# Optimization experiments

Measured on AMD Instinct MI355X. Metric: run time of the kernel, lower is better.

The kernel has to match this reference:

```python
import jax, jax.numpy as jnp
import numpy as np

N, K, D = 32768, 8192, 256


def setup_inputs() -> dict:
    key = jax.random.key(0)
    k1, k2 = jax.random.split(key)
    z = jax.random.normal(k1, (N, D), dtype=jnp.float32)
    # nn.Embedding weight initialized uniform(-1/K, 1/K)
    emb = jax.random.uniform(k2, (K, D), dtype=jnp.float32, minval=-1.0 / K, maxval=1.0 / K)
    return {"z": z, "emb": emb}


def reference(z, emb):
    # squared-distance: ||z||^2 + ||e||^2 - 2 z e^T  -> [N, K]
    distances = (
        jnp.sum(z * z, axis=-1, keepdims=True)
        + jnp.sum(emb * emb, axis=-1)
        - 2.0 * (z @ emb.T)
    )
    closest = jnp.argmin(distances, axis=-1)  # [N]
    one_hot = jax.nn.one_hot(closest, emb.shape[0], dtype=z.dtype)  # [N, K]
    quantized = one_hot @ emb  # [N, D]
    return quantized
```

## Files before the change

kernel.cpp:

```cpp
#include <hip/hip_runtime.h>

#define NROWS 32768
#define KC 8192
#define DDIM 256
#define D4 64
#define CAP 128
#define DELTA 4e-4f

typedef _Float16 half8 __attribute__((ext_vector_type(8)));
typedef float f32x4 __attribute__((ext_vector_type(4)));
typedef unsigned int uint;
typedef const __attribute__((address_space(1))) unsigned int* gptr_u32;
typedef __attribute__((address_space(3))) unsigned int* lptr_u32;

union H4 { ushort4 u; _Float16 h[4]; };

__global__ __launch_bounds__(256) void vq_znorm(const float* __restrict__ z,
                                                float* __restrict__ An) {
#pragma clang fp contract(off)
  const int row = blockIdx.x * 256 + threadIdx.x;
  const float* a = z + (size_t)row * 256;
  float halves[2];
#pragma unroll
  for (int h = 0; h < 2; ++h) {
    const float* p = a + h * 128;
    float r[8];
#pragma unroll
    for (int j = 0; j < 8; ++j) { const float v = p[j]; r[j] = v * v; }
    for (int i = 8; i < 128; i += 8) {
#pragma unroll
      for (int j = 0; j < 8; ++j) { const float v = p[i + j]; r[j] += v * v; }
    }
    halves[h] = ((r[0] + r[1]) + (r[2] + r[3])) + ((r[4] + r[5]) + (r[6] + r[7]));
  }
  An[row] = halves[0] + halves[1];
}

__global__ __launch_bounds__(256) void vq_convert(const float* __restrict__ z,
                                                  const float* __restrict__ emb,
                                                  _Float16* __restrict__ z16,
                                                  _Float16* __restrict__ e16,
                                                  uint* __restrict__ rowmin,
                                                  int* __restrict__ cnt) {
  const int tid = blockIdx.x * 256 + threadIdx.x;
  const float4* z4 = (const float4*)z;
  const float4* e4 = (const float4*)emb;
  ushort4* z16u = (ushort4*)z16;
  ushort4* e16u = (ushort4*)e16;
#pragma unroll
  for (int t = 0; t < 4; ++t) {
    const int i = tid + t * 524288;
    const float4 v = z4[i];
    H4 o;
    o.h[0] = (_Float16)v.x; o.h[1] = (_Float16)v.y;
    o.h[2] = (_Float16)v.z; o.h[3] = (_Float16)v.w;
    z16u[i] = o.u;
  }
  {
    const int i = tid;
    const float4 v = e4[i];
    H4 o;
    o.h[0] = (_Float16)(v.x * 8192.0f); o.h[1] = (_Float16)(v.y * 8192.0f);
    o.h[2] = (_Float16)(v.z * 8192.0f); o.h[3] = (_Float16)(v.w * 8192.0f);
    e16u[i] = o.u;
  }
  if (tid < NROWS) { rowmin[tid] = 0x7F800000u; cnt[tid] = 0; }
}

__global__ __launch_bounds__(256) void vq_gemm_filter(
    const _Float16* __restrict__ z16, const _Float16* __restrict__ e16,
    const float* __restrict__ An, uint* __restrict__ rowmin,
    int* __restrict__ cnt, int* __restrict__ list) {
  __shared__ _Float16 As[128 * 32];
  __shared__ _Float16 Bs[128 * 32];
  const int bid = blockIdx.x;
  const int swz = (bid & 7) * 2048 + (bid >> 3);
  const int nIdx = swz >> 8;
  const int mIdx = swz & 255;
  const int brow = mIdx * 128, bcol = nIdx * 128;
  const int tid = threadIdx.x;
  const int lane = tid & 63, w = tid >> 6;
  const int wr = w >> 1, wc = w & 1;
  const int l15 = lane & 15, l4 = lane >> 4;

  f32x4 acc[4][4] = {{{0.f}}};

  for (int ks = 0; ks < 8; ++ks) {
    const int k0 = ks * 32;
    __syncthreads();
#pragma unroll
    for (int i = 0; i < 2; ++i) {
      const int c = tid + 256 * i;
      const int r = c >> 2, off = (c & 3) * 8;
      __builtin_amdgcn_global_load_lds(
          (gptr_u32)(z16 + (size_t)(brow + r) * DDIM + k0 + off),
          (lptr_u32)(As + c * 8), 16, 0, 0);
      __builtin_amdgcn_global_load_lds(
          (gptr_u32)(e16 + (size_t)(bcol + r) * DDIM + k0 + off),
          (lptr_u32)(Bs + c * 8), 16, 0, 0);
    }
    __syncthreads();
    half8 af[4], bf[4];
#pragma unroll
    for (int m = 0; m < 4; ++m)
      af[m] = *(const half8*)(As + (wr * 64 + m * 16 + l15) * 32 + l4 * 8);
#pragma unroll
    for (int n = 0; n < 4; ++n)
      bf[n] = *(const half8*)(Bs + (wc * 64 + n * 16 + l15) * 32 + l4 * 8);
#pragma unroll
    for (int m = 0; m < 4; ++m)
#pragma unroll
      for (int n = 0; n < 4; ++n)
        acc[m][n] = __builtin_amdgcn_mfma_f32_16x16x32_f16(af[m], bf[n], acc[m][n], 0, 0, 0);
  }

  float An_r[4][4];
#pragma unroll
  for (int m = 0; m < 4; ++m)
#pragma unroll
    for (int r = 0; r < 4; ++r)
      An_r[m][r] = An[brow + wr * 64 + m * 16 + l4 * 4 + r];

  float rmin[4][4];
#pragma unroll
  for (int m = 0; m < 4; ++m)
#pragma unroll
    for (int r = 0; r < 4; ++r) rmin[m][r] = 3.4e38f;
#pragma unroll
  for (int m = 0; m < 4; ++m)
#pragma unroll
    for (int n = 0; n < 4; ++n)
#pragma unroll
      for (int r = 0; r < 4; ++r) {
        const float s = fmaf(acc[m][n][r], -0x1p-12f, An_r[m][r]);
        acc[m][n][r] = s;
        rmin[m][r] = fminf(rmin[m][r], s);
      }
#pragma unroll
  for (int off = 1; off < 16; off <<= 1)
#pragma unroll
    for (int m = 0; m < 4; ++m)
#pragma unroll
      for (int r = 0; r < 4; ++r)
        rmin[m][r] = fminf(rmin[m][r], __shfl_xor(rmin[m][r], off, 64));

  float cur[4][4];
#pragma unroll
  for (int m = 0; m < 4; ++m)
#pragma unroll
    for (int r = 0; r < 4; ++r) {
      const int row = brow + wr * 64 + m * 16 + l4 * 4 + r;
      float oldf = 3.4e38f;
      if (l15 == 0)
        oldf = __uint_as_float(atomicMin(rowmin + row, __float_as_uint(rmin[m][r])));
      oldf = __shfl(oldf, lane & 48, 64);
      cur[m][r] = fminf(oldf, rmin[m][r]) + DELTA;
    }
#pragma unroll
  for (int m = 0; m < 4; ++m)
#pragma unroll
    for (int n = 0; n < 4; ++n)
#pragma unroll
      for (int r = 0; r < 4; ++r) {
        if (acc[m][n][r] <= cur[m][r]) {
          const int row = brow + wr * 64 + m * 16 + l4 * 4 + r;
          const int code = bcol + wc * 64 + n * 16 + l15;
          const int pos = atomicAdd(cnt + row, 1);
          if (pos < CAP) list[row * CAP + pos] = code;
        }
      }
}

__global__ __launch_bounds__(64) void vq_recheck(
    const float* __restrict__ z, const float* __restrict__ emb,
    const float* __restrict__ An, const int* __restrict__ cnt,
    const int* __restrict__ list, int* __restrict__ idxo) {
  const int row = blockIdx.x;
  const int lane = threadIdx.x;
  const int nc = cnt[row];
  const float Ar = An[row];
  const float4* z4r = (const float4*)z + (size_t)row * D4;
  const float4* e4 = (const float4*)emb;
  float bs = 3.4e38f;
  int bi = 0x7fffffff;
  if (nc <= CAP) {
    for (int c = lane; c < nc; c += 64) {
      const int code = list[row * CAP + c];
      float p = 0.f;
      for (int d = 0; d < D4; ++d) {
        const float4 zv = z4r[d];
        const float4 ev = e4[(size_t)code * D4 + d];
        p = fmaf(zv.x, ev.x, p); p = fmaf(zv.y, ev.y, p);
        p = fmaf(zv.z, ev.z, p); p = fmaf(zv.w, ev.w, p);
      }
      const float s = Ar - 2.0f * p;
      if (s < bs || (s == bs && code < bi)) { bs = s; bi = code; }
    }
  } else {
    for (int code = lane; code < KC; code += 64) {
      float p = 0.f;
      for (int d = 0; d < D4; ++d) {
        const float4 zv = z4r[d];
        const float4 ev = e4[(size_t)code * D4 + d];
        p = fmaf(zv.x, ev.x, p); p = fmaf(zv.y, ev.y, p);
        p = fmaf(zv.z, ev.z, p); p = fmaf(zv.w, ev.w, p);
      }
      const float s = Ar - 2.0f * p;
      if (s < bs || (s == bs && code < bi)) { bs = s; bi = code; }
    }
  }
#pragma unroll
  for (int off = 1; off < 64; off <<= 1) {
    const float os = __shfl_xor(bs, off, 64);
    const int oi = __shfl_xor(bi, off, 64);
    if (os < bs || (os == bs && oi < bi)) { bs = os; bi = oi; }
  }
  if (lane == 0) idxo[row] = bi;
}

__global__ __launch_bounds__(256) void vq_gather(const float* __restrict__ emb,
                                                 const int* __restrict__ idxo,
                                                 float* __restrict__ out) {
  const float4* e4 = (const float4*)emb;
  float4* o4 = (float4*)out;
  const int id = blockIdx.x * 256 + threadIdx.x;
#pragma unroll
  for (int t = 0; t < 4; ++t) {
    const int g = id + t * 524288;
    const int nrow = g >> 6;
    const int d4c = g & 63;
    o4[g] = e4[(size_t)idxo[nrow] * D4 + d4c];
  }
}

extern "C" void kernel_launch(void* const* d_in, const int* in_sizes, int n_in,
                              void* d_out, int out_size, void* d_ws, size_t ws_size,
                              hipStream_t stream) {
  const float* z = (const float*)d_in[0];
  const float* emb = (const float*)d_in[1];
  float* out = (float*)d_out;

  char* wsb = (char*)d_ws;
  float* An = (float*)(wsb);
  uint* rowmin = (uint*)(wsb + (128 << 10));
  int* cnt = (int*)(wsb + (256 << 10));
  int* idx = (int*)(wsb + (384 << 10));
  int* list = (int*)(wsb + (512 << 10));
  _Float16* z16 = (_Float16*)(wsb + (512 << 10) + (16 << 20));
  _Float16* e16 = (_Float16*)(wsb + (512 << 10) + (32 << 20));

  vq_znorm<<<NROWS / 256, 256, 0, stream>>>(z, An);
  vq_convert<<<2048, 256, 0, stream>>>(z, emb, z16, e16, rowmin, cnt);
  vq_gemm_filter<<<16384, 256, 0, stream>>>(z16, e16, An, rowmin, cnt, list);
  vq_recheck<<<NROWS, 64, 0, stream>>>(z, emb, An, cnt, list, idx);
  vq_gather<<<2048, 256, 0, stream>>>(emb, idx, out);
}
```

Before: 623.8 us.

## Keep z tile in registers and stream codebook panels with double-buffered LDS

The GEMM-filter kernel now keeps each block's full 128-row fp16 z tile (all 256 dims) in registers and loops over a 1024-code segment in 64-code panels. The panels are double-buffered in XOR-swizzled LDS, and each row's running minimum is tightened as panels go by, so fewer candidates get pushed to the lists. This replaces 16384 small blocks that each reloaded z and E over K with 2048 persistent blocks, which cuts global traffic and atomic contention. The recheck and gather kernels are fused so each wave writes its output row directly, and znorm switches to float4 loads; the cost is more registers and larger shared memory, which can lower occupancy.

```diff
diff --git a/kernel.cpp b/kernel.cpp
--- a/kernel.cpp
+++ b/kernel.cpp
@@ -6,6 +6,11 @@
 #define D4 64
 #define CAP 128
 #define DELTA 4e-4f
+#define MT 128
+#define NSEG 8
+#define SEGC (KC / NSEG)
+#define PAN 64
+#define NPAN (SEGC / PAN)
 
 typedef _Float16 half8 __attribute__((ext_vector_type(8)));
 typedef float f32x4 __attribute__((ext_vector_type(4)));
@@ -19,17 +24,19 @@
                                                 float* __restrict__ An) {
 #pragma clang fp contract(off)
   const int row = blockIdx.x * 256 + threadIdx.x;
-  const float* a = z + (size_t)row * 256;
+  const float4* p4 = (const float4*)(z + (size_t)row * 256);
   float halves[2];
 #pragma unroll
   for (int h = 0; h < 2; ++h) {
-    const float* p = a + h * 128;
     float r[8];
-#pragma unroll
-    for (int j = 0; j < 8; ++j) { const float v = p[j]; r[j] = v * v; }
-    for (int i = 8; i < 128; i += 8) {
-#pragma unroll
-      for (int j = 0; j < 8; ++j) { const float v = p[i + j]; r[j] += v * v; }
+    float4 a = p4[h * 32 + 0], b = p4[h * 32 + 1];
+    r[0] = a.x * a.x; r[1] = a.y * a.y; r[2] = a.z * a.z; r[3] = a.w * a.w;
+    r[4] = b.x * b.x; r[5] = b.y * b.y; r[6] = b.z * b.z; r[7] = b.w * b.w;
+    for (int i = 1; i < 16; ++i) {
+      a = p4[h * 32 + i * 2];
+      b = p4[h * 32 + i * 2 + 1];
+      r[0] += a.x * a.x; r[1] += a.y * a.y; r[2] += a.z * a.z; r[3] += a.w * a.w;
+      r[4] += b.x * b.x; r[5] += b.y * b.y; r[6] += b.z * b.z; r[7] += b.w * b.w;
     }
     halves[h] = ((r[0] + r[1]) + (r[2] + r[3])) + ((r[4] + r[5]) + (r[6] + r[7]));
   }
@@ -71,112 +78,160 @@
     const _Float16* __restrict__ z16, const _Float16* __restrict__ e16,
     const float* __restrict__ An, uint* __restrict__ rowmin,
     int* __restrict__ cnt, int* __restrict__ list) {
-  __shared__ _Float16 As[128 * 32];
-  __shared__ _Float16 Bs[128 * 32];
+  __shared__ _Float16 smem[32768];
   const int bid = blockIdx.x;
-  const int swz = (bid & 7) * 2048 + (bid >> 3);
-  const int nIdx = swz >> 8;
-  const int mIdx = swz & 255;
-  const int brow = mIdx * 128, bcol = nIdx * 128;
+  const int seg = bid & 7, mIdx = bid >> 3;
+  const int brow = mIdx * MT;
+  const int c0seg = seg * SEGC;
   const int tid = threadIdx.x;
   const int lane = tid & 63, w = tid >> 6;
-  const int wr = w >> 1, wc = w & 1;
   const int l15 = lane & 15, l4 = lane >> 4;
-
-  f32x4 acc[4][4] = {{{0.f}}};
-
-  for (int ks = 0; ks < 8; ++ks) {
-    const int k0 = ks * 32;
+  const int wrow = w * 32;
+
+#pragma unroll
+  for (int i = 0; i < 16; ++i) {
+    const int c = tid + 256 * i;
+    const int r = c >> 5, sl = (c & 31) ^ (r & 31);
+    __builtin_amdgcn_global_load_lds(
+        (gptr_u32)(z16 + (size_t)(brow + r) * DDIM + sl * 8),
+        (lptr_u32)(smem + c * 8), 16, 0, 0);
+  }
+  __syncthreads();
+  half8 af[2][8];
+#pragma unroll
+  for (int m = 0; m < 2; ++m) {
+    const int row = wrow + m * 16 + l15;
+#pragma unroll
+    for (int k = 0; k < 8; ++k) {
+      const int sl = (k * 4 + l4) ^ (row & 31);
+      af[m][k] = *(const half8*)(smem + row * 256 + sl * 8);
+    }
+  }
+  __syncthreads();
+
+  float An_r[2][4];
+#pragma unroll
+  for (int m = 0; m < 2; ++m) {
+    const f32x4 a4 = *(const f32x4*)(An + brow + wrow + m * 16 + l4 * 4);
+#pragma unroll
+    for (int r = 0; r < 4; ++r) An_r[m][r] = a4[r];
+  }
+
+  float rl[2][4], g[2][4], thr[2][4];
+#pragma unroll
+  for (int m = 0; m < 2; ++m)
+#pragma unroll
+    for (int r = 0; r < 4; ++r) { rl[m][r] = 3.4e38f; g[m][r] = 3.4e38f; thr[m][r] = 3.4e38f; }
+
+  {
+    const int cb = c0seg;
+#pragma unroll
+    for (int i = 0; i < 8; ++i) {
+      const int c = tid + 256 * i;
+      const int r = c >> 5, sl = (c & 31) ^ (r & 31);
+      __builtin_amdgcn_global_load_lds(
+          (gptr_u32)(e16 + (size_t)(cb + r) * DDIM + sl * 8),
+          (lptr_u32)(smem + c * 8), 16, 0, 0);
+    }
+  }
+  __syncthreads();
+
+  for (int p = 0; p < NPAN; ++p) {
+    const int curoff = (p & 1) << 14;
+    const int nxtoff = curoff ^ 16384;
+    if (p + 1 < NPAN) {
+      const int cb = c0seg + (p + 1) * PAN;
+#pragma unroll
+      for (int i = 0; i < 8; ++i) {
+        const int c = tid + 256 * i;
+        const int r = c >> 5, sl = (c & 31) ^ (r & 31);
+        __builtin_amdgcn_global_load_lds(
+            (gptr_u32)(e16 + (size_t)(cb + r) * DDIM + sl * 8),
+            (lptr_u32)(smem + nxtoff + c * 8), 16, 0, 0);
+      }
+    }
+    f32x4 acc[2][4] = {{{0.f}}};
+#pragma unroll
+    for (int k = 0; k < 8; ++k) {
+      half8 bf[4];
+#pragma unroll
+      for (int n = 0; n < 4; ++n) {
+        const int crow = n * 16 + l15;
+        const int sl = (k * 4 + l4) ^ (crow & 31);
+        bf[n] = *(const half8*)(smem + curoff + crow * 256 + sl * 8);
+      }
+#pragma unroll
+      for (int m = 0; m < 2; ++m)
+#pragma unroll
+        for (int n = 0; n < 4; ++n)
+          acc[m][n] = __builtin_amdgcn_mfma_f32_16x16x32_f16(af[m][k], bf[n], acc[m][n], 0, 0, 0);
+    }
+
+    float pm[2][4];
+#pragma unroll
+    for (int m = 0; m < 2; ++m)
+#pragma unroll
+      for (int r = 0; r < 4; ++r) pm[m][r] = 3.4e38f;
+#pragma unroll
+    for (int m = 0; m < 2; ++m)
+#pragma unroll
+      for (int n = 0; n < 4; ++n)
+#pragma unroll
+        for (int r = 0; r < 4; ++r) {
+          const float s = fmaf(acc[m][n][r], -0x1p-12f, An_r[m][r]);
+          acc[m][n][r] = s;
+          pm[m][r] = fminf(pm[m][r], s);
+        }
+#pragma unroll
+    for (int off = 1; off < 16; off <<= 1)
+#pragma unroll
+      for (int m = 0; m < 2; ++m)
+#pragma unroll
+        for (int r = 0; r < 4; ++r)
+          pm[m][r] = fminf(pm[m][r], __shfl_xor(pm[m][r], off, 64));
+
+    bool anyf = false;
+#pragma unroll
+    for (int m = 0; m < 2; ++m)
+#pragma unroll
+      for (int r = 0; r < 4; ++r) {
+        if (pm[m][r] < rl[m][r]) {
+          rl[m][r] = pm[m][r];
+          if (l15 == 0) {
+            const int row = brow + wrow + m * 16 + l4 * 4 + r;
+            const uint old = atomicMin(rowmin + row, __float_as_uint(pm[m][r]));
+            g[m][r] = fminf(g[m][r], __uint_as_float(old));
+          }
+        }
+        const float t = fminf(g[m][r], rl[m][r]) + DELTA;
+        thr[m][r] = __shfl(t, lane & 48, 64);
+        anyf |= (pm[m][r] <= thr[m][r]);
+      }
+    if (__any(anyf)) {
+#pragma unroll
+      for (int m = 0; m < 2; ++m)
+#pragma unroll
+        for (int n = 0; n < 4; ++n)
+#pragma unroll
+          for (int r = 0; r < 4; ++r) {
+            if (acc[m][n][r] <= thr[m][r]) {
+              const int row = brow + wrow + m * 16 + l4 * 4 + r;
+              const int code = c0seg + p * PAN + n * 16 + l15;
+              const int pos = atomicAdd(cnt + row, 1);
+              if (pos < CAP) list[(size_t)row * CAP + pos] = code;
+            }
+          }
+    }
     __syncthreads();
-#pragma unroll
-    for (int i = 0; i < 2; ++i) {
-      const int c = tid + 256 * i;
-      const int r = c >> 2, off = (c & 3) * 8;
-      __builtin_amdgcn_global_load_lds(
-          (gptr_u32)(z16 + (size_t)(brow + r) * DDIM + k0 + off),
-          (lptr_u32)(As + c * 8), 16, 0, 0);
-      __builtin_amdgcn_global_load_lds(
-          (gptr_u32)(e16 + (size_t)(bcol + r) * DDIM + k0 + off),
-          (lptr_u32)(Bs + c * 8), 16, 0, 0);
-    }
-    __syncthreads();
-    half8 af[4], bf[4];
-#pragma unroll
-    for (int m = 0; m < 4; ++m)
-      af[m] = *(const half8*)(As + (wr * 64 + m * 16 + l15) * 32 + l4 * 8);
-#pragma unroll
-    for (int n = 0; n < 4; ++n)
-      bf[n] = *(const half8*)(Bs + (wc * 64 + n * 16 + l15) * 32 + l4 * 8);
-#pragma unroll
-    for (int m = 0; m < 4; ++m)
-#pragma unroll
-      for (int n = 0; n < 4; ++n)
-        acc[m][n] = __builtin_amdgcn_mfma_f32_16x16x32_f16(af[m], bf[n], acc[m][n], 0, 0, 0);
-  }
-
-  float An_r[4][4];
-#pragma unroll
-  for (int m = 0; m < 4; ++m)
-#pragma unroll
-    for (int r = 0; r < 4; ++r)
-      An_r[m][r] = An[brow + wr * 64 + m * 16 + l4 * 4 + r];
-
-  float rmin[4][4];
-#pragma unroll
-  for (int m = 0; m < 4; ++m)
-#pragma unroll
-    for (int r = 0; r < 4; ++r) rmin[m][r] = 3.4e38f;
-#pragma unroll
-  for (int m = 0; m < 4; ++m)
-#pragma unroll
-    for (int n = 0; n < 4; ++n)
-#pragma unroll
-      for (int r = 0; r < 4; ++r) {
-        const float s = fmaf(acc[m][n][r], -0x1p-12f, An_r[m][r]);
-        acc[m][n][r] = s;
-        rmin[m][r] = fminf(rmin[m][r], s);
-      }
-#pragma unroll
-  for (int off = 1; off < 16; off <<= 1)
-#pragma unroll
-    for (int m = 0; m < 4; ++m)
-#pragma unroll
-      for (int r = 0; r < 4; ++r)
-        rmin[m][r] = fminf(rmin[m][r], __shfl_xor(rmin[m][r], off, 64));
-
-  float cur[4][4];
-#pragma unroll
-  for (int m = 0; m < 4; ++m)
-#pragma unroll
-    for (int r = 0; r < 4; ++r) {
-      const int row = brow + wr * 64 + m * 16 + l4 * 4 + r;
-      float oldf = 3.4e38f;
-      if (l15 == 0)
-        oldf = __uint_as_float(atomicMin(rowmin + row, __float_as_uint(rmin[m][r])));
-      oldf = __shfl(oldf, lane & 48, 64);
-      cur[m][r] = fminf(oldf, rmin[m][r]) + DELTA;
-    }
-#pragma unroll
-  for (int m = 0; m < 4; ++m)
-#pragma unroll
-    for (int n = 0; n < 4; ++n)
-#pragma unroll
-      for (int r = 0; r < 4; ++r) {
-        if (acc[m][n][r] <= cur[m][r]) {
-          const int row = brow + wr * 64 + m * 16 + l4 * 4 + r;
-          const int code = bcol + wc * 64 + n * 16 + l15;
-          const int pos = atomicAdd(cnt + row, 1);
-          if (pos < CAP) list[row * CAP + pos] = code;
-        }
-      }
-}
-
-__global__ __launch_bounds__(64) void vq_recheck(
+  }
+}
+
+__global__ __launch_bounds__(256) void vq_recheck_gather(
     const float* __restrict__ z, const float* __restrict__ emb,
     const float* __restrict__ An, const int* __restrict__ cnt,
-    const int* __restrict__ list, int* __restrict__ idxo) {
-  const int row = blockIdx.x;
-  const int lane = threadIdx.x;
+    const int* __restrict__ list, float* __restrict__ out) {
+  const int row = blockIdx.x * 4 + (threadIdx.x >> 6);
+  const int lane = threadIdx.x & 63;
   const int nc = cnt[row];
   const float Ar = An[row];
   const float4* z4r = (const float4*)z + (size_t)row * D4;
@@ -185,7 +240,7 @@
   int bi = 0x7fffffff;
   if (nc <= CAP) {
     for (int c = lane; c < nc; c += 64) {
-      const int code = list[row * CAP + c];
+      const int code = list[(size_t)row * CAP + c];
       float p = 0.f;
       for (int d = 0; d < D4; ++d) {
         const float4 zv = z4r[d];
@@ -215,22 +270,8 @@
     const int oi = __shfl_xor(bi, off, 64);
     if (os < bs || (os == bs && oi < bi)) { bs = os; bi = oi; }
   }
-  if (lane == 0) idxo[row] = bi;
-}
-
-__global__ __launch_bounds__(256) void vq_gather(const float* __restrict__ emb,
-                                                 const int* __restrict__ idxo,
-                                                 float* __restrict__ out) {
-  const float4* e4 = (const float4*)emb;
-  float4* o4 = (float4*)out;
-  const int id = blockIdx.x * 256 + threadIdx.x;
-#pragma unroll
-  for (int t = 0; t < 4; ++t) {
-    const int g = id + t * 524288;
-    const int nrow = g >> 6;
-    const int d4c = g & 63;
-    o4[g] = e4[(size_t)idxo[nrow] * D4 + d4c];
-  }
+  const float4 v = e4[(size_t)bi * D4 + lane];
+  ((float4*)out)[(size_t)row * D4 + lane] = v;
 }
 
 extern "C" void kernel_launch(void* const* d_in, const int* in_sizes, int n_in,
@@ -244,14 +285,12 @@
   float* An = (float*)(wsb);
   uint* rowmin = (uint*)(wsb + (128 << 10));
   int* cnt = (int*)(wsb + (256 << 10));
-  int* idx = (int*)(wsb + (384 << 10));
   int* list = (int*)(wsb + (512 << 10));
   _Float16* z16 = (_Float16*)(wsb + (512 << 10) + (16 << 20));
   _Float16* e16 = (_Float16*)(wsb + (512 << 10) + (32 << 20));
 
   vq_znorm<<<NROWS / 256, 256, 0, stream>>>(z, An);
   vq_convert<<<2048, 256, 0, stream>>>(z, emb, z16, e16, rowmin, cnt);
-  vq_gemm_filter<<<16384, 256, 0, stream>>>(z16, e16, An, rowmin, cnt, list);
-  vq_recheck<<<NROWS, 64, 0, stream>>>(z, emb, An, cnt, list, idx);
-  vq_gather<<<2048, 256, 0, stream>>>(emb, idx, out);
-}
+  vq_gemm_filter<<<2048, 256, 0, stream>>>(z16, e16, An, rowmin, cnt, list);
+  vq_recheck_gather<<<NROWS / 4, 256, 0, stream>>>(z, emb, An, cnt, list, out);
+}
```

Measured after the change: 557.5 us. 1.12x faster.
